# Kernel tuning notes

Hardware: AMD Instinct MI355X
Metric: run time of the kernel (lower is better)

Reference implementation:

```python
import jax, jax.numpy as jnp
import numpy as np

B_, K_, D_, L_, N_, R_ = 2, 4, 128, 4096, 16, 8


def setup_inputs() -> dict:
    key = jax.random.key(0)
    ks = jax.random.split(key, 7)
    return {
        "q_x": jax.random.normal(ks[0], (B_, K_, D_, L_), jnp.float32),
        "kv_x": jax.random.normal(ks[1], (B_, K_, D_, L_), jnp.float32),
        "x_proj_weight": jax.random.normal(ks[2], (K_, R_ + 2 * N_, D_), jnp.float32) * 0.02,
        "dt_projs_weight": jax.random.normal(ks[3], (K_, D_, R_), jnp.float32) * 0.02,
        "dt_projs_bias": jax.random.normal(ks[4], (K_, D_), jnp.float32) * 0.1,
        "A_logs": jax.random.uniform(ks[5], (K_ * D_, N_), jnp.float32),
        "Ds": jax.random.normal(ks[6], (K_ * D_,), jnp.float32),
    }


def _selective_scan(u, delta, A, Bmat, Cmat, Ds):
    # u, delta: [B,K,D,L]; A: [K,D,N]; Bmat, Cmat: [B,K,N,L]; Ds: [K,D]
    uT = jnp.moveaxis(u, -1, 0)      # [L,B,K,D]
    dT = jnp.moveaxis(delta, -1, 0)  # [L,B,K,D]
    BT = jnp.moveaxis(Bmat, -1, 0)   # [L,B,K,N]
    CT = jnpp if False else jnp.moveaxis(Cmat, -1, 0)  # [L,B,K,N]
    h0 = jnp.zeros(u.shape[:3] + (A.shape[-1],), jnp.float32)  # [B,K,D,N]

    def step(h, xs):
        u_l, d_l, B_l, C_l = xs
        dA = jnp.exp(d_l[..., None] * A)  # [B,K,D,N]
        h = dA * h + (d_l * u_l)[..., None] * B_l[:, :, None, :]
        y = jnp.einsum('bkdn,bkn->bkd', h, C_l)
        return h, y

    _, yT = jax.lax.scan(step, h0, (uT, dT, BT, CT))
    y = jnp.moveaxis(yT, 0, -1)  # [B,K,D,L]
    return y + u * Ds[None, :, :, None]


def reference(q_x, kv_x, x_proj_weight, dt_projs_weight, dt_projs_bias, A_logs, Ds):
    B, K, D, L = kv_x.shape
    N = A_logs.shape[1]
    R = dt_projs_weight.shape[2]
    # projections of kv (for dt, B) and q (for C)
    x_dbl = jnp.einsum('bkdl,kcd->bkcl', kv_x, x_proj_weight)
    x_c = jnp.einsum('bkdl,kcd->bkcl', q_x, x_proj_weight)
    dts = x_dbl[:, :, :R]          # [B,K,R,L]
    Bs = x_dbl[:, :, R:R + N]      # [B,K,N,L]
    Cs = x_c[:, :, R + N:]         # [B,K,N,L]
    dts = jnp.einsum('bkrl,kdr->bkdl', dts, dt_projs_weight)
    A = -jnp.exp(A_logs.astype(jnp.float32)).reshape(K, D, N)
    delta = jax.nn.softplus(dts.astype(jnp.float32) + dt_projs_bias.astype(jnp.float32)[None, :, :, None])
    y = _selective_scan(kv_x.astype(jnp.float32), delta, A,
                        Bs.astype(jnp.float32), Cs.astype(jnp.float32),
                        Ds.astype(jnp.float32).reshape(K, D))
    return y  # [B,K,D,L] float32
```

## Files before the change

kernel.cpp:

```cpp
#include <hip/hip_runtime.h>
#include <cmath>

namespace {
constexpr int B_ = 2, K_ = 4, D_ = 128, L_ = 4096, N_ = 16, R_ = 8, C_ = 40;
constexpr int CHUNK = 32, NCH = L_ / CHUNK;
constexpr float LOG2E = 1.44269504f;
}

#if __has_builtin(__builtin_amdgcn_exp2f)
#define FEXP2(x) __builtin_amdgcn_exp2f(x)
#else
#define FEXP2(x) exp2f(x)
#endif

__global__ __launch_bounds__(640, 2) void k1_proj(
    const float* __restrict__ qx, const float* __restrict__ kv,
    const float* __restrict__ xw,
    float* __restrict__ dtsT, float* __restrict__ BT, float* __restrict__ CT)
{
    __shared__ float Wt[D_ * C_];

    const int tid = threadIdx.x;
    const int w = tid >> 6, lane = tid & 63;
    const int dg = lane >> 5, lq = lane & 31;
    int blk = blockIdx.x;
    const int lt = blk & 31; blk >>= 5;
    const int k = blk & 3; const int b = blk >> 2;
    const int bk = b * K_ + k;

    for (int i = tid; i < C_ * D_; i += 640) {
        const int c = i >> 7, d = i & 127;
        Wt[d * C_ + c] = xw[(k * C_ + c) * D_ + d];
    }
    __syncthreads();

    const float* xsrc = (w >= 6) ? qx : kv;
    const int c0 = w * 4;
    float acc[4][4];
    #pragma unroll
    for (int c = 0; c < 4; ++c)
        #pragma unroll
        for (int j = 0; j < 4; ++j) acc[c][j] = 0.f;

    const float* src = xsrc + ((size_t)bk * D_ + dg * 64) * L_ + lt * 128 + 4 * lq;
    #pragma unroll 16
    for (int dd = 0; dd < 64; ++dd) {
        const float4 x = *(const float4*)(src + (size_t)dd * L_);
        const float4 wv = *(const float4*)&Wt[(dg * 64 + dd) * C_ + c0];
        const float* wp = (const float*)&wv;
        #pragma unroll
        for (int c = 0; c < 4; ++c) {
            acc[c][0] = fmaf(x.x, wp[c], acc[c][0]);
            acc[c][1] = fmaf(x.y, wp[c], acc[c][1]);
            acc[c][2] = fmaf(x.z, wp[c], acc[c][2]);
            acc[c][3] = fmaf(x.w, wp[c], acc[c][3]);
        }
    }

    #pragma unroll
    for (int c = 0; c < 4; ++c)
        #pragma unroll
        for (int j = 0; j < 4; ++j)
            acc[c][j] += __shfl_xor(acc[c][j], 32, 64);

    #pragma unroll
    for (int jj = 0; jj < 2; ++jj) {
        const int j = dg * 2 + jj;
        const int l = lt * 128 + 4 * lq + j;
        float4 o; o.x = acc[0][j]; o.y = acc[1][j]; o.z = acc[2][j]; o.w = acc[3][j];
        if (w < 2)
            *(float4*)(dtsT + ((size_t)bk * L_ + l) * R_ + w * 4) = o;
        else if (w < 6)
            *(float4*)(BT + ((size_t)bk * L_ + l) * N_ + (w - 2) * 4) = o;
        else
            *(float4*)(CT + ((size_t)bk * L_ + l) * N_ + (w - 6) * 4) = o;
    }
}

__global__ __launch_bounds__(128, 1) void k2_pass1(
    const float* __restrict__ kv, const float* __restrict__ dtsT,
    const float* __restrict__ BT, const float* __restrict__ alg,
    const float* __restrict__ dtw, const float* __restrict__ dtb,
    float* __restrict__ hend, float* __restrict__ Ssum)
{
    __shared__ float dts_s[CHUNK * R_];
    __shared__ float B_s[CHUNK * N_];

    const int tid = threadIdx.x;
    const int d = tid;
    const int blk = blockIdx.x;
    const int ch = blk & (NCH - 1);
    const int bk = blk >> 7;
    const int k = bk & 3;

    {
        const float* src = dtsT + ((size_t)bk * L_ + ch * CHUNK) * R_;
        if (tid < 64) *(float4*)&dts_s[4 * tid] = *(const float4*)(src + 4 * tid);
        const float* bsrc = BT + ((size_t)bk * L_ + ch * CHUNK) * N_;
        *(float4*)&B_s[4 * tid] = *(const float4*)(bsrc + 4 * tid);
    }

    float uu[CHUNK];
    {
        const float4* up = (const float4*)(kv + ((size_t)bk * D_ + d) * L_ + ch * CHUNK);
        #pragma unroll
        for (int j = 0; j < 8; ++j) {
            const float4 v = up[j];
            uu[4*j] = v.x; uu[4*j+1] = v.y; uu[4*j+2] = v.z; uu[4*j+3] = v.w;
        }
    }

    float dtwr[R_];
    {
        const float* p = dtw + ((size_t)k * D_ + d) * R_;
        *(float4*)&dtwr[0] = *(const float4*)p;
        *(float4*)&dtwr[4] = *(const float4*)(p + 4);
    }
    const float bias = dtb[k * D_ + d];
    float A2[N_];
    {
        const float* ap = alg + ((size_t)k * D_ + d) * N_;
        #pragma unroll
        for (int j = 0; j < 4; ++j) {
            float4 a = *(const float4*)(ap + 4 * j);
            A2[4*j]   = -__expf(a.x) * LOG2E; A2[4*j+1] = -__expf(a.y) * LOG2E;
            A2[4*j+2] = -__expf(a.z) * LOG2E; A2[4*j+3] = -__expf(a.w) * LOG2E;
        }
    }
    __syncthreads();

    float h[N_];
    #pragma unroll
    for (int n = 0; n < N_; ++n) h[n] = 0.f;
    float sd = 0.f;

    #pragma unroll
    for (int l = 0; l < CHUNK; ++l) {
        float dv[R_];
        *(float4*)&dv[0] = *(const float4*)&dts_s[l * R_];
        *(float4*)&dv[4] = *(const float4*)&dts_s[l * R_ + 4];
        float s = bias;
        #pragma unroll
        for (int r = 0; r < R_; ++r) s = fmaf(dv[r], dtwr[r], s);
        const float e = FEXP2(s * LOG2E);
        const float dlt = (s > 15.f) ? s : __logf(1.f + e);
        sd += dlt;
        const float xb = dlt * uu[l];
        #pragma unroll
        for (int g = 0; g < 4; ++g) {
            const float4 bg = *(const float4*)&B_s[l * N_ + 4 * g];
            h[4*g+0] = fmaf(FEXP2(dlt * A2[4*g+0]), h[4*g+0], xb * bg.x);
            h[4*g+1] = fmaf(FEXP2(dlt * A2[4*g+1]), h[4*g+1], xb * bg.y);
            h[4*g+2] = fmaf(FEXP2(dlt * A2[4*g+2]), h[4*g+2], xb * bg.z);
            h[4*g+3] = fmaf(FEXP2(dlt * A2[4*g+3]), h[4*g+3], xb * bg.w);
        }
    }

    float* hp = hend + (((size_t)bk * NCH + ch) * D_ + d) * N_;
    #pragma unroll
    for (int j = 0; j < 4; ++j) {
        float4 o; o.x = h[4*j]; o.y = h[4*j+1]; o.z = h[4*j+2]; o.w = h[4*j+3];
        *(float4*)(hp + 4 * j) = o;
    }
    Ssum[((size_t)bk * NCH + ch) * D_ + d] = sd;
}

__global__ __launch_bounds__(64, 2) void k25_chain(
    const float* __restrict__ alg, const float* __restrict__ Ssum,
    const float* __restrict__ hend, float* __restrict__ hinit)
{
    const int tg = blockIdx.x * 64 + threadIdx.x;
    const int n = tg & 15;
    const int d = (tg >> 4) & 127;
    const int bk = tg >> 11;
    const int k = bk & 3;

    const float A2 = -__expf(alg[((size_t)k * D_ + d) * N_ + n]) * LOG2E;
    float h = 0.f;
    for (int c0 = 0; c0 < NCH; c0 += 32) {
        float he[32], ss[32];
        #pragma unroll
        for (int j = 0; j < 32; ++j) {
            const size_t si = ((size_t)bk * NCH + c0 + j) * D_ + d;
            he[j] = hend[si * N_ + n];
            ss[j] = Ssum[si];
        }
        #pragma unroll
        for (int j = 0; j < 32; ++j) {
            const size_t si = ((size_t)bk * NCH + c0 + j) * D_ + d;
            hinit[si * N_ + n] = h;
            h = fmaf(FEXP2(ss[j] * A2), h, he[j]);
        }
    }
}

__global__ __launch_bounds__(128, 1) void k3_pass2(
    const float* __restrict__ kv, const float* __restrict__ dtsT,
    const float* __restrict__ BT, const float* __restrict__ CT,
    const float* __restrict__ alg, const float* __restrict__ dtw,
    const float* __restrict__ dtb, const float* __restrict__ DsG,
    const float* __restrict__ hinit, float* __restrict__ out)
{
    __shared__ float dts_s[CHUNK * R_];
    __shared__ float B_s[CHUNK * N_];
    __shared__ float C_s[CHUNK * N_];
    const int tid = threadIdx.x;
    const int d = tid;
    const int blk = blockIdx.x;
    const int ch = blk & (NCH - 1);
    const int bk = blk >> 7;
    const int k = bk & 3;

    {
        const float* src = dtsT + ((size_t)bk * L_ + ch * CHUNK) * R_;
        if (tid < 64) *(float4*)&dts_s[4 * tid] = *(const float4*)(src + 4 * tid);
        const float* bsrc = BT + ((size_t)bk * L_ + ch * CHUNK) * N_;
        *(float4*)&B_s[4 * tid] = *(const float4*)(bsrc + 4 * tid);
        const float* csrc = CT + ((size_t)bk * L_ + ch * CHUNK) * N_;
        *(float4*)&C_s[4 * tid] = *(const float4*)(csrc + 4 * tid);
    }
    float uu[CHUNK];
    {
        const float4* up = (const float4*)(kv + ((size_t)bk * D_ + d) * L_ + ch * CHUNK);
        #pragma unroll
        for (int j = 0; j < 8; ++j) {
            const float4 v = up[j];
            uu[4*j] = v.x; uu[4*j+1] = v.y; uu[4*j+2] = v.z; uu[4*j+3] = v.w;
        }
    }
    float dtwr[R_];
    {
        const float* p = dtw + ((size_t)k * D_ + d) * R_;
        *(float4*)&dtwr[0] = *(const float4*)p;
        *(float4*)&dtwr[4] = *(const float4*)(p + 4);
    }
    const float bias = dtb[k * D_ + d];
    const float Dv = DsG[k * D_ + d];
    float A2[N_];
    {
        const float* ap = alg + ((size_t)k * D_ + d) * N_;
        #pragma unroll
        for (int j = 0; j < 4; ++j) {
            float4 a = *(const float4*)(ap + 4 * j);
            A2[4*j]   = -__expf(a.x) * LOG2E; A2[4*j+1] = -__expf(a.y) * LOG2E;
            A2[4*j+2] = -__expf(a.z) * LOG2E; A2[4*j+3] = -__expf(a.w) * LOG2E;
        }
    }
    float h[N_];
    {
        const float* hp = hinit + (((size_t)bk * NCH + ch) * D_ + d) * N_;
        #pragma unroll
        for (int j = 0; j < 4; ++j) {
            float4 v = *(const float4*)(hp + 4 * j);
            h[4*j] = v.x; h[4*j+1] = v.y; h[4*j+2] = v.z; h[4*j+3] = v.w;
        }
    }
    __syncthreads();

    float* orow = out + ((size_t)bk * D_ + d) * L_ + ch * CHUNK;
    float4 yv;
    #pragma unroll
    for (int l = 0; l < CHUNK; ++l) {
        float dv[R_];
        *(float4*)&dv[0] = *(const float4*)&dts_s[l * R_];
        *(float4*)&dv[4] = *(const float4*)&dts_s[l * R_ + 4];
        float s = bias;
        #pragma unroll
        for (int r = 0; r < R_; ++r) s = fmaf(dv[r], dtwr[r], s);
        const float e = FEXP2(s * LOG2E);
        const float dlt = (s > 15.f) ? s : __logf(1.f + e);
        const float xb = dlt * uu[l];
        float p0 = 0.f, p1 = 0.f;
        #pragma unroll
        for (int g = 0; g < 4; ++g) {
            const float4 bg = *(const float4*)&B_s[l * N_ + 4 * g];
            const float4 cg4 = *(const float4*)&C_s[l * N_ + 4 * g];
            h[4*g+0] = fmaf(FEXP2(dlt * A2[4*g+0]), h[4*g+0], xb * bg.x);
            p0 = fmaf(h[4*g+0], cg4.x, p0);
            h[4*g+1] = fmaf(FEXP2(dlt * A2[4*g+1]), h[4*g+1], xb * bg.y);
            p1 = fmaf(h[4*g+1], cg4.y, p1);
            h[4*g+2] = fmaf(FEXP2(dlt * A2[4*g+2]), h[4*g+2], xb * bg.z);
            p0 = fmaf(h[4*g+2], cg4.z, p0);
            h[4*g+3] = fmaf(FEXP2(dlt * A2[4*g+3]), h[4*g+3], xb * bg.w);
            p1 = fmaf(h[4*g+3], cg4.w, p1);
        }
        ((float*)&yv)[l & 3] = fmaf(uu[l], Dv, p0 + p1);
        if ((l & 3) == 3) *(float4*)(orow + (l - 3)) = yv;
    }
}

extern "C" void kernel_launch(void* const* d_in, const int* in_sizes, int n_in,
                              void* d_out, int out_size, void* d_ws, size_t ws_size,
                              hipStream_t stream)
{
    const float* qx  = (const float*)d_in[0];
    const float* kv  = (const float*)d_in[1];
    const float* xw  = (const float*)d_in[2];
    const float* dtw = (const float*)d_in[3];
    const float* dtb = (const float*)d_in[4];
    const float* alg = (const float*)d_in[5];
    const float* Ds  = (const float*)d_in[6];
    float* out = (float*)d_out;

    const size_t sz_dts = (size_t)B_ * K_ * L_ * R_;
    const size_t sz_bc  = (size_t)B_ * K_ * L_ * N_;
    const size_t sz_h   = (size_t)B_ * K_ * NCH * D_ * N_;
    const size_t sz_ss  = (size_t)B_ * K_ * NCH * D_;
    const size_t need = (sz_dts + 2 * sz_bc + 2 * sz_h + sz_ss) * sizeof(float);
    if (ws_size < need) return;

    float* dts   = (float*)d_ws;
    float* BTp   = dts + sz_dts;
    float* CTp   = BTp + sz_bc;
    float* hend  = CTp + sz_bc;
    float* hinit = hend + sz_h;
    float* Ssm   = hinit + sz_h;

    k1_proj<<<B_ * K_ * 32, 640, 0, stream>>>(qx, kv, xw, dts, BTp, CTp);
    k2_pass1<<<B_ * K_ * NCH, 128, 0, stream>>>(kv, dts, BTp, alg, dtw, dtb, hend, Ssm);
    k25_chain<<<256, 64, 0, stream>>>(alg, Ssm, hend, hinit);
    k3_pass2<<<B_ * K_ * NCH, 128, 0, stream>>>(kv, dts, BTp, CTp, alg, dtw, dtb, Ds, hinit, out);
}
```

Before: 69.80 us.

## Split state dimension across two threads per channel and stage u/y through LDS

Scan kernels now use two threads per d channel, each handling 8 of the 16 state entries, doubling the thread count to 256 and cutting per-thread register use. The u chunk is loaded cooperatively with coalesced float4 reads into padded shared memory, and outputs are reduced with a lane shuffle, staged in LDS, and written back coalesced. k1 now writes all four outputs from the dg==0 half and uses a smaller unroll. This costs a duplicated softplus/dt computation per thread pair and adds LDS traffic in exchange for more parallelism and better memory coalescing.

```diff
diff --git a/kernel.cpp b/kernel.cpp
--- a/kernel.cpp
+++ b/kernel.cpp
@@ -4,6 +4,7 @@
 namespace {
 constexpr int B_ = 2, K_ = 4, D_ = 128, L_ = 4096, N_ = 16, R_ = 8, C_ = 40;
 constexpr int CHUNK = 32, NCH = L_ / CHUNK;
+constexpr int US = CHUNK + 1;
 constexpr float LOG2E = 1.44269504f;
 }
 
@@ -43,7 +44,7 @@
         for (int j = 0; j < 4; ++j) acc[c][j] = 0.f;
 
     const float* src = xsrc + ((size_t)bk * D_ + dg * 64) * L_ + lt * 128 + 4 * lq;
-    #pragma unroll 16
+    #pragma unroll 8
     for (int dd = 0; dd < 64; ++dd) {
         const float4 x = *(const float4*)(src + (size_t)dd * L_);
         const float4 wv = *(const float4*)&Wt[(dg * 64 + dd) * C_ + c0];
@@ -63,51 +64,54 @@
         for (int j = 0; j < 4; ++j)
             acc[c][j] += __shfl_xor(acc[c][j], 32, 64);
 
-    #pragma unroll
-    for (int jj = 0; jj < 2; ++jj) {
-        const int j = dg * 2 + jj;
-        const int l = lt * 128 + 4 * lq + j;
-        float4 o; o.x = acc[0][j]; o.y = acc[1][j]; o.z = acc[2][j]; o.w = acc[3][j];
-        if (w < 2)
-            *(float4*)(dtsT + ((size_t)bk * L_ + l) * R_ + w * 4) = o;
-        else if (w < 6)
-            *(float4*)(BT + ((size_t)bk * L_ + l) * N_ + (w - 2) * 4) = o;
-        else
-            *(float4*)(CT + ((size_t)bk * L_ + l) * N_ + (w - 6) * 4) = o;
-    }
-}
-
-__global__ __launch_bounds__(128, 1) void k2_pass1(
+    if (dg == 0) {
+        #pragma unroll
+        for (int j = 0; j < 4; ++j) {
+            const int l = lt * 128 + 4 * lq + j;
+            float4 o; o.x = acc[0][j]; o.y = acc[1][j]; o.z = acc[2][j]; o.w = acc[3][j];
+            if (w < 2)
+                *(float4*)(dtsT + ((size_t)bk * L_ + l) * R_ + w * 4) = o;
+            else if (w < 6)
+                *(float4*)(BT + ((size_t)bk * L_ + l) * N_ + (w - 2) * 4) = o;
+            else
+                *(float4*)(CT + ((size_t)bk * L_ + l) * N_ + (w - 6) * 4) = o;
+        }
+    }
+}
+
+__global__ __launch_bounds__(256, 4) void k2_pass1(
     const float* __restrict__ kv, const float* __restrict__ dtsT,
     const float* __restrict__ BT, const float* __restrict__ alg,
     const float* __restrict__ dtw, const float* __restrict__ dtb,
     float* __restrict__ hend, float* __restrict__ Ssum)
 {
+    __shared__ float u_s[D_ * US];
     __shared__ float dts_s[CHUNK * R_];
     __shared__ float B_s[CHUNK * N_];
 
     const int tid = threadIdx.x;
-    const int d = tid;
+    const int d = tid >> 1, nh = tid & 1;
     const int blk = blockIdx.x;
     const int ch = blk & (NCH - 1);
     const int bk = blk >> 7;
     const int k = bk & 3;
 
     {
+        const float* base = kv + ((size_t)bk * D_) * L_ + ch * CHUNK;
+        #pragma unroll
+        for (int p = 0; p < 4; ++p) {
+            const int f = tid + p * 256;
+            const int row = f >> 3, c4 = (f & 7) * 4;
+            const float4 v = *(const float4*)(base + (size_t)row * L_ + c4);
+            float* pp = &u_s[row * US + c4];
+            pp[0] = v.x; pp[1] = v.y; pp[2] = v.z; pp[3] = v.w;
+        }
+    }
+    {
         const float* src = dtsT + ((size_t)bk * L_ + ch * CHUNK) * R_;
         if (tid < 64) *(float4*)&dts_s[4 * tid] = *(const float4*)(src + 4 * tid);
         const float* bsrc = BT + ((size_t)bk * L_ + ch * CHUNK) * N_;
-        *(float4*)&B_s[4 * tid] = *(const float4*)(bsrc + 4 * tid);
-    }
-
-    float uu[CHUNK];
-    {
-        const float4* up = (const float4*)(kv + ((size_t)bk * D_ + d) * L_ + ch * CHUNK);
-        #pragma unroll
-        for (int j = 0; j < 8; ++j) {
-            const float4 v = up[j];
-            uu[4*j] = v.x; uu[4*j+1] = v.y; uu[4*j+2] = v.z; uu[4*j+3] = v.w;
-        }
+        if (tid < 128) *(float4*)&B_s[4 * tid] = *(const float4*)(bsrc + 4 * tid);
     }
 
     float dtwr[R_];
@@ -117,11 +121,11 @@
         *(float4*)&dtwr[4] = *(const float4*)(p + 4);
     }
     const float bias = dtb[k * D_ + d];
-    float A2[N_];
-    {
-        const float* ap = alg + ((size_t)k * D_ + d) * N_;
-        #pragma unroll
-        for (int j = 0; j < 4; ++j) {
+    float A2[8];
+    {
+        const float* ap = alg + ((size_t)k * D_ + d) * N_ + nh * 8;
+        #pragma unroll
+        for (int j = 0; j < 2; ++j) {
             float4 a = *(const float4*)(ap + 4 * j);
             A2[4*j]   = -__expf(a.x) * LOG2E; A2[4*j+1] = -__expf(a.y) * LOG2E;
             A2[4*j+2] = -__expf(a.z) * LOG2E; A2[4*j+3] = -__expf(a.w) * LOG2E;
@@ -129,9 +133,9 @@
     }
     __syncthreads();
 
-    float h[N_];
-    #pragma unroll
-    for (int n = 0; n < N_; ++n) h[n] = 0.f;
+    float h[8];
+    #pragma unroll
+    for (int n = 0; n < 8; ++n) h[n] = 0.f;
     float sd = 0.f;
 
     #pragma unroll
@@ -145,10 +149,10 @@
         const float e = FEXP2(s * LOG2E);
         const float dlt = (s > 15.f) ? s : __logf(1.f + e);
         sd += dlt;
-        const float xb = dlt * uu[l];
-        #pragma unroll
-        for (int g = 0; g < 4; ++g) {
-            const float4 bg = *(const float4*)&B_s[l * N_ + 4 * g];
+        const float xb = dlt * u_s[d * US + l];
+        #pragma unroll
+        for (int g = 0; g < 2; ++g) {
+            const float4 bg = *(const float4*)&B_s[l * N_ + nh * 8 + 4 * g];
             h[4*g+0] = fmaf(FEXP2(dlt * A2[4*g+0]), h[4*g+0], xb * bg.x);
             h[4*g+1] = fmaf(FEXP2(dlt * A2[4*g+1]), h[4*g+1], xb * bg.y);
             h[4*g+2] = fmaf(FEXP2(dlt * A2[4*g+2]), h[4*g+2], xb * bg.z);
@@ -156,13 +160,14 @@
         }
     }
 
-    float* hp = hend + (((size_t)bk * NCH + ch) * D_ + d) * N_;
-    #pragma unroll
-    for (int j = 0; j < 4; ++j) {
-        float4 o; o.x = h[4*j]; o.y = h[4*j+1]; o.z = h[4*j+2]; o.w = h[4*j+3];
-        *(float4*)(hp + 4 * j) = o;
-    }
-    Ssum[((size_t)bk * NCH + ch) * D_ + d] = sd;
+    float* hp = hend + (((size_t)bk * NCH + ch) * D_ + d) * N_ + nh * 8;
+    {
+        float4 o0; o0.x = h[0]; o0.y = h[1]; o0.z = h[2]; o0.w = h[3];
+        float4 o1; o1.x = h[4]; o1.y = h[5]; o1.z = h[6]; o1.w = h[7];
+        *(float4*)hp = o0;
+        *(float4*)(hp + 4) = o1;
+    }
+    if (nh == 0) Ssum[((size_t)bk * NCH + ch) * D_ + d] = sd;
 }
 
 __global__ __launch_bounds__(64, 2) void k25_chain(
@@ -194,40 +199,46 @@
     }
 }
 
-__global__ __launch_bounds__(128, 1) void k3_pass2(
+__global__ __launch_bounds__(256, 4) void k3_pass2(
     const float* __restrict__ kv, const float* __restrict__ dtsT,
     const float* __restrict__ BT, const float* __restrict__ CT,
     const float* __restrict__ alg, const float* __restrict__ dtw,
     const float* __restrict__ dtb, const float* __restrict__ DsG,
     const float* __restrict__ hinit, float* __restrict__ out)
 {
+    __shared__ float u_s[D_ * US];
+    __shared__ float y_s[D_ * US];
     __shared__ float dts_s[CHUNK * R_];
     __shared__ float B_s[CHUNK * N_];
     __shared__ float C_s[CHUNK * N_];
+
     const int tid = threadIdx.x;
-    const int d = tid;
+    const int d = tid >> 1, nh = tid & 1;
     const int blk = blockIdx.x;
     const int ch = blk & (NCH - 1);
     const int bk = blk >> 7;
     const int k = bk & 3;
 
     {
+        const float* base = kv + ((size_t)bk * D_) * L_ + ch * CHUNK;
+        #pragma unroll
+        for (int p = 0; p < 4; ++p) {
+            const int f = tid + p * 256;
+            const int row = f >> 3, c4 = (f & 7) * 4;
+            const float4 v = *(const float4*)(base + (size_t)row * L_ + c4);
+            float* pp = &u_s[row * US + c4];
+            pp[0] = v.x; pp[1] = v.y; pp[2] = v.z; pp[3] = v.w;
+        }
+    }
+    {
         const float* src = dtsT + ((size_t)bk * L_ + ch * CHUNK) * R_;
         if (tid < 64) *(float4*)&dts_s[4 * tid] = *(const float4*)(src + 4 * tid);
         const float* bsrc = BT + ((size_t)bk * L_ + ch * CHUNK) * N_;
-        *(float4*)&B_s[4 * tid] = *(const float4*)(bsrc + 4 * tid);
         const float* csrc = CT + ((size_t)bk * L_ + ch * CHUNK) * N_;
-        *(float4*)&C_s[4 * tid] = *(const float4*)(csrc + 4 * tid);
-    }
-    float uu[CHUNK];
-    {
-        const float4* up = (const float4*)(kv + ((size_t)bk * D_ + d) * L_ + ch * CHUNK);
-        #pragma unroll
-        for (int j = 0; j < 8; ++j) {
-            const float4 v = up[j];
-            uu[4*j] = v.x; uu[4*j+1] = v.y; uu[4*j+2] = v.z; uu[4*j+3] = v.w;
-        }
-    }
+        if (tid < 128) *(float4*)&B_s[4 * tid] = *(const float4*)(bsrc + 4 * tid);
+        else           *(float4*)&C_s[4 * (tid - 128)] = *(const float4*)(csrc + 4 * (tid - 128));
+    }
+
     float dtwr[R_];
     {
         const float* p = dtw + ((size_t)k * D_ + d) * R_;
@@ -236,29 +247,26 @@
     }
     const float bias = dtb[k * D_ + d];
     const float Dv = DsG[k * D_ + d];
-    float A2[N_];
-    {
-        const float* ap = alg + ((size_t)k * D_ + d) * N_;
-        #pragma unroll
-        for (int j = 0; j < 4; ++j) {
+    float A2[8];
+    {
+        const float* ap = alg + ((size_t)k * D_ + d) * N_ + nh * 8;
+        #pragma unroll
+        for (int j = 0; j < 2; ++j) {
             float4 a = *(const float4*)(ap + 4 * j);
             A2[4*j]   = -__expf(a.x) * LOG2E; A2[4*j+1] = -__expf(a.y) * LOG2E;
             A2[4*j+2] = -__expf(a.z) * LOG2E; A2[4*j+3] = -__expf(a.w) * LOG2E;
         }
     }
-    float h[N_];
-    {
-        const float* hp = hinit + (((size_t)bk * NCH + ch) * D_ + d) * N_;
-        #pragma unroll
-        for (int j = 0; j < 4; ++j) {
-            float4 v = *(const float4*)(hp + 4 * j);
-            h[4*j] = v.x; h[4*j+1] = v.y; h[4*j+2] = v.z; h[4*j+3] = v.w;
-        }
+    float h[8];
+    {
+        const float* hp = hinit + (((size_t)bk * NCH + ch) * D_ + d) * N_ + nh * 8;
+        float4 v0 = *(const float4*)hp;
+        float4 v1 = *(const float4*)(hp + 4);
+        h[0] = v0.x; h[1] = v0.y; h[2] = v0.z; h[3] = v0.w;
+        h[4] = v1.x; h[5] = v1.y; h[6] = v1.z; h[7] = v1.w;
     }
     __syncthreads();
 
-    float* orow = out + ((size_t)bk * D_ + d) * L_ + ch * CHUNK;
-    float4 yv;
     #pragma unroll
     for (int l = 0; l < CHUNK; ++l) {
         float dv[R_];
@@ -269,12 +277,13 @@
         for (int r = 0; r < R_; ++r) s = fmaf(dv[r], dtwr[r], s);
         const float e = FEXP2(s * LOG2E);
         const float dlt = (s > 15.f) ? s : __logf(1.f + e);
-        const float xb = dlt * uu[l];
+        const float ul = u_s[d * US + l];
+        const float xb = dlt * ul;
         float p0 = 0.f, p1 = 0.f;
         #pragma unroll
-        for (int g = 0; g < 4; ++g) {
-            const float4 bg = *(const float4*)&B_s[l * N_ + 4 * g];
-            const float4 cg4 = *(const float4*)&C_s[l * N_ + 4 * g];
+        for (int g = 0; g < 2; ++g) {
+            const float4 bg  = *(const float4*)&B_s[l * N_ + nh * 8 + 4 * g];
+            const float4 cg4 = *(const float4*)&C_s[l * N_ + nh * 8 + 4 * g];
             h[4*g+0] = fmaf(FEXP2(dlt * A2[4*g+0]), h[4*g+0], xb * bg.x);
             p0 = fmaf(h[4*g+0], cg4.x, p0);
             h[4*g+1] = fmaf(FEXP2(dlt * A2[4*g+1]), h[4*g+1], xb * bg.y);
@@ -284,8 +293,19 @@
             h[4*g+3] = fmaf(FEXP2(dlt * A2[4*g+3]), h[4*g+3], xb * bg.w);
             p1 = fmaf(h[4*g+3], cg4.w, p1);
         }
-        ((float*)&yv)[l & 3] = fmaf(uu[l], Dv, p0 + p1);
-        if ((l & 3) == 3) *(float4*)(orow + (l - 3)) = yv;
+        float p = p0 + p1;
+        p += __shfl_xor(p, 1, 64);
+        if (nh == 0) y_s[d * US + l] = fmaf(ul, Dv, p);
+    }
+    __syncthreads();
+
+    #pragma unroll
+    for (int p = 0; p < 4; ++p) {
+        const int f = tid + p * 256;
+        const int row = f >> 3, j4 = (f & 7) * 4;
+        const float* yp = &y_s[row * US + j4];
+        float4 o; o.x = yp[0]; o.y = yp[1]; o.z = yp[2]; o.w = yp[3];
+        *(float4*)(out + ((size_t)bk * D_ + row) * L_ + ch * CHUNK + j4) = o;
     }
 }
 
@@ -317,7 +337,7 @@
     float* Ssm   = hinit + sz_h;
 
     k1_proj<<<B_ * K_ * 32, 640, 0, stream>>>(qx, kv, xw, dts, BTp, CTp);
-    k2_pass1<<<B_ * K_ * NCH, 128, 0, stream>>>(kv, dts, BTp, alg, dtw, dtb, hend, Ssm);
+    k2_pass1<<<B_ * K_ * NCH, 256, 0, stream>>>(kv, dts, BTp, alg, dtw, dtb, hend, Ssm);
     k25_chain<<<256, 64, 0, stream>>>(alg, Ssm, hend, hinit);
-    k3_pass2<<<B_ * K_ * NCH, 128, 0, stream>>>(kv, dts, BTp, CTp, alg, dtw, dtb, Ds, hinit, out);
-}
+    k3_pass2<<<B_ * K_ * NCH, 256, 0, stream>>>(kv, dts, BTp, CTp, alg, dtw, dtb, Ds, hinit, out);
+}
```

New measurement: 68.62 us. No clear change (-1.7%).
